# Optimization experiments

Measured on AMD Instinct MI355X. Metric: run time of the kernel, lower is better.

The kernel has to match this reference:

```python
import jax, jax.numpy as jnp
import numpy as np

T, B, IN = 1000, 64, 300          # timesteps, batch, input neurons
A, P = 6, 4                        # num_areas, pop_per_area
L = A * P                          # latent_size = 24
O = 200                            # neurons per area (n_units=1200 / 6 areas)
N_DELAY = 5                        # effective recurrent synaptic delay (steps)
SIGMA = 0.1                        # sigma_mem_noise
TAU = 10.0


def setup_inputs() -> dict:
    key = jax.random.key(0)
    ks = jax.random.split(key, 8)
    x = jax.random.normal(ks[0], (T, B, IN), jnp.float32)
    mem_noise = jax.random.normal(ks[1], (T, B, L), jnp.float32)
    trial_noise = jax.random.uniform(ks[2], (B, 2), jnp.float32) - 0.5
    w_in = jax.random.normal(ks[3], (L, IN), jnp.float32) / np.sqrt(IN)
    w_rec = jax.random.normal(ks[4], (1, L, L), jnp.float32) / np.sqrt(L)
    v_rest = jnp.zeros((L,), jnp.float32)
    bias_noise = jnp.ones((L,), jnp.float32)
    trial_offset_w = (jax.random.uniform(ks[5], (2, L), jnp.float32) - 0.5) / np.sqrt(2.0)
    decay_v = jnp.full((L,), np.exp(-1.0 / TAU), jnp.float32)
    proj_w = jax.random.normal(ks[6], (A, O, P), jnp.float32) / np.sqrt(P)
    proj_b = jnp.zeros((A, O), jnp.float32)
    return dict(x=x, mem_noise=mem_noise, trial_noise=trial_noise, w_in=w_in,
                w_rec=w_rec, v_rest=v_rest, bias_noise=bias_noise,
                trial_offset_w=trial_offset_w, decay_v=decay_v,
                proj_w=proj_w, proj_b=proj_b)


def reference(x, mem_noise, trial_noise, w_in, w_rec, v_rest, bias_noise,
              trial_offset_w, decay_v, proj_w, proj_b):
    # Constant-per-trial offset + input current + resting potential: (T,B,L)
    offset = trial_noise @ trial_offset_w                       # (B,L)
    drive = jnp.einsum('tbi,li->tbl', x, w_in) + offset + v_rest
    noise = SIGMA * bias_noise * mem_noise                      # (T,B,L)
    w_rec0_t = w_rec[0].T                                       # (L,L)

    def step(carry, inp):
        v, buf = carry                 # buf: (N_DELAY,B,L), oldest first
        d, n = inp
        i_rec = buf[0] @ w_rec0_t      # delayed population rate -> current
        v = decay_v * v + (1.0 - decay_v) * (d + i_rec) + n
        rate = jax.nn.sigmoid(v)       # population firing rate
        buf = jnp.concatenate([buf[1:], rate[None]], axis=0)
        return (v, buf), rate

    v0 = jnp.zeros((B, L), x.dtype)
    buf0 = jnp.zeros((N_DELAY, B, L), x.dtype)
    _, rates = jax.lax.scan(step, (v0, buf0), (drive, noise))   # (T,B,L)

    # Per-area projection from population rates to per-neuron rates.
    pop = rates.reshape(T, B, A, P)
    units = jnp.einsum('tbap,aop->tbao', pop, proj_w) + proj_b  # (T,B,A,O)
    return jax.nn.sigmoid(units).reshape(T, B, A * O)
```

## Files before the change

kernel.cpp:

```cpp
#include <hip/hip_runtime.h>

#define T_STEPS 1000
#define BATCH   64
#define IN_N    300
#define L_N     24
#define SIGMA   0.1f
#define RSTR    32

typedef float f32x4 __attribute__((ext_vector_type(4)));

#define WS_G_OFF  8192
#define TBL       (T_STEPS * BATCH * L_N)

__global__ void k0_prep(const float* __restrict__ w_in, const float* __restrict__ w_rec,
                        const float* __restrict__ v_rest, const float* __restrict__ bias_noise,
                        const float* __restrict__ trial_offset_w, const float* __restrict__ decay_v,
                        float* __restrict__ ws) {
    int i = blockIdx.x * 256 + threadIdx.x;
    float* wTs = ws;
    float* Wss = ws + 7200;
    float* ow  = ws + 7776;
    float* c0  = ws + 7824;
    float* snl = ws + 7848;
    if (i < 7200) {
        int k = i / 24, l = i % 24;
        wTs[i] = w_in[l * 300 + k] * (1.f - decay_v[l]);
    } else if (i < 7776) {
        int j = i - 7200; int l = j / 24;
        Wss[j] = w_rec[j] * (1.f - decay_v[l]);
    } else if (i < 7824) {
        int j = i - 7776; int l = j % 24;
        ow[j] = trial_offset_w[j] * (1.f - decay_v[l]);
    } else if (i < 7848) {
        int l = i - 7824;
        c0[l] = v_rest[l] * (1.f - decay_v[l]);
    } else if (i < 7872) {
        int l = i - 7848;
        snl[l] = SIGMA * bias_noise[l];
    }
}

#define K1_ROWS    128
#define K1_THREADS 128
#define KC         60
#define XPITCH     61

__global__ __launch_bounds__(K1_THREADS) void k1_drive(
    const float* __restrict__ x, const float* __restrict__ ws,
    const float* __restrict__ trial_noise, const float* __restrict__ mem_noise,
    float* __restrict__ g) {
    __shared__ float xt[K1_ROWS * XPITCH];
    const float* wTs = ws;
    const float* ow  = ws + 7776;
    const float* c0  = ws + 7824;
    const float* snl = ws + 7848;
    const int tid  = threadIdx.x;
    const int row0 = blockIdx.x * K1_ROWS;

    float acc[L_N];
#pragma unroll
    for (int l = 0; l < L_N; ++l) acc[l] = 0.f;

    const float4* xg = reinterpret_cast<const float4*>(x);
    for (int c = 0; c < IN_N / KC; ++c) {
#pragma unroll
        for (int j = 0; j < 15; ++j) {
            int e4 = tid + j * K1_THREADS;
            int r = e4 / 15, kq = e4 % 15;
            float4 v = xg[(row0 + r) * (IN_N / 4) + c * (KC / 4) + kq];
            float* d = &xt[r * XPITCH + kq * 4];
            d[0] = v.x; d[1] = v.y; d[2] = v.z; d[3] = v.w;
        }
        __syncthreads();
        const float* wrow = wTs + c * KC * L_N;
#pragma unroll 2
        for (int kk = 0; kk < KC; ++kk) {
            float xv = xt[tid * XPITCH + kk];
#pragma unroll
            for (int l = 0; l < L_N; ++l)
                acc[l] = fmaf(xv, wrow[kk * L_N + l], acc[l]);
        }
        __syncthreads();
    }

    const int row = row0 + tid;
    const int b   = row & (BATCH - 1);
    float2 tn = reinterpret_cast<const float2*>(trial_noise)[b];
    const float4* nz = reinterpret_cast<const float4*>(mem_noise + (size_t)row * L_N);
    float4 z[6];
#pragma unroll
    for (int q = 0; q < 6; ++q) z[q] = nz[q];
    float zz[L_N];
#pragma unroll
    for (int q = 0; q < 6; ++q) {
        zz[4*q] = z[q].x; zz[4*q+1] = z[q].y; zz[4*q+2] = z[q].z; zz[4*q+3] = z[q].w;
    }
    float o[L_N];
#pragma unroll
    for (int l = 0; l < L_N; ++l)
        o[l] = acc[l] + tn.x * ow[l] + tn.y * ow[L_N + l] + c0[l] + snl[l] * zz[l];
    float4* dg = reinterpret_cast<float4*>(g + (size_t)row * L_N);
#pragma unroll
    for (int i = 0; i < 6; ++i)
        dg[i] = make_float4(o[4*i], o[4*i+1], o[4*i+2], o[4*i+3]);
}

#define K2_STEP(s, C0, C1, C2, CG) do {                                        \
    float p0 = C0.x * W0.x, p1 = C0.y * W0.y, p2 = C0.z * W0.z, p3 = C0.w * W0.w; \
    p0 = fmaf(C1.x, W1.x, p0); p1 = fmaf(C1.y, W1.y, p1);                      \
    p2 = fmaf(C1.z, W1.z, p2); p3 = fmaf(C1.w, W1.w, p3);                      \
    p0 = fmaf(C2.x, W2.x, p0); p1 = fmaf(C2.y, W2.y, p1);                      \
    p2 = fmaf(C2.z, W2.z, p2); p3 = fmaf(C2.w, W2.w, p3);                      \
    { const float4* q_ = reinterpret_cast<const float4*>(                      \
          &ring[(((s) + 5) & 7) * RSTR + h12]);                                \
      C0 = q_[0]; C1 = q_[1]; C2 = q_[2]; }                                    \
    float pa = (p0 + p1) + (p2 + p3);                                          \
    pa += __shfl_xor(pa, 32);                                                  \
    v = fmaf(dec, v, (CG) + pa);                                               \
    float rate_ = 1.f / (1.f + __expf(-v));                                    \
    if (act) {                                                                 \
        ring[((s) & 7) * RSTR + li] = rate_;                                   \
        rp[(tb + (s)) * (BATCH * L_N)] = rate_;                                \
    }                                                                          \
} while (0)

__global__ __launch_bounds__(64) void k2_scan(
    const float* __restrict__ g, const float* __restrict__ ws,
    const float* __restrict__ decay_v, float* __restrict__ rates) {
    __shared__ __align__(16) float ring[8 * RSTR];
    const float* Wss = ws + 7200;
    const int tid  = threadIdx.x;
    const int b    = blockIdx.x;
    const int half = tid >> 5;
    const int li   = tid & 31;
    const int lc   = (li < 24) ? li : 0;
    const bool act = (li < 24) && (half == 0);
    const int h12  = half * 12;

    const float4* wv = reinterpret_cast<const float4*>(Wss + lc * 24 + h12);
    float4 W0 = wv[0], W1 = wv[1], W2 = wv[2];
    const float dec = decay_v[lc];

    ring[tid] = 0.f; ring[tid + 64] = 0.f; ring[tid + 128] = 0.f; ring[tid + 192] = 0.f;
    __syncthreads();

    const float* gp = g + b * L_N + lc;
    float* rp = rates + b * L_N + lc;

    float cg0 = gp[0 * 1536], cg1 = gp[1 * 1536], cg2 = gp[2 * 1536], cg3 = gp[3 * 1536];
    float cg4 = gp[4 * 1536], cg5 = gp[5 * 1536], cg6 = gp[6 * 1536], cg7 = gp[7 * 1536];

    float v = 0.f;
    float4 A0, A1, A2, B0, B1, B2;
    {
        const float4* q = reinterpret_cast<const float4*>(&ring[3 * RSTR + h12]);
        A0 = q[0]; A1 = q[1]; A2 = q[2];
        q = reinterpret_cast<const float4*>(&ring[4 * RSTR + h12]);
        B0 = q[0]; B1 = q[1]; B2 = q[2];
    }

    for (int tb = 0; tb < T_STEPS - 8; tb += 8) {
        const float* gn = gp + (tb + 8) * 1536;
        float n0 = gn[0 * 1536], n1 = gn[1 * 1536], n2 = gn[2 * 1536], n3 = gn[3 * 1536];
        float n4 = gn[4 * 1536], n5 = gn[5 * 1536], n6 = gn[6 * 1536], n7 = gn[7 * 1536];
        K2_STEP(0, A0, A1, A2, cg0);
        K2_STEP(1, B0, B1, B2, cg1);
        K2_STEP(2, A0, A1, A2, cg2);
        K2_STEP(3, B0, B1, B2, cg3);
        K2_STEP(4, A0, A1, A2, cg4);
        K2_STEP(5, B0, B1, B2, cg5);
        K2_STEP(6, A0, A1, A2, cg6);
        K2_STEP(7, B0, B1, B2, cg7);
        cg0 = n0; cg1 = n1; cg2 = n2; cg3 = n3;
        cg4 = n4; cg5 = n5; cg6 = n6; cg7 = n7;
    }
    {
        const int tb = T_STEPS - 8;
        K2_STEP(0, A0, A1, A2, cg0);
        K2_STEP(1, B0, B1, B2, cg1);
        K2_STEP(2, A0, A1, A2, cg2);
        K2_STEP(3, B0, B1, B2, cg3);
        K2_STEP(4, A0, A1, A2, cg4);
        K2_STEP(5, B0, B1, B2, cg5);
        K2_STEP(6, A0, A1, A2, cg6);
        K2_STEP(7, B0, B1, B2, cg7);
    }
}

#define K3_ROWS 32
__global__ __launch_bounds__(320) void k3_proj(
    const float* __restrict__ rates, const float* __restrict__ proj_w,
    const float* __restrict__ proj_b, float* __restrict__ out) {
    __shared__ float4 lw[1200];
    __shared__ float4 lb[300];
    __shared__ float4 lp[K3_ROWS * 6];
    const int tid  = threadIdx.x;
    const int row0 = blockIdx.x * K3_ROWS;

    const float4* pw4 = reinterpret_cast<const float4*>(proj_w);
    const float4* pb4 = reinterpret_cast<const float4*>(proj_b);
    const float4* rt4 = reinterpret_cast<const float4*>(rates);
    for (int i = tid; i < 1200; i += 320) lw[i] = pw4[i];
    if (tid < 300) lb[tid] = pb4[tid];
    if (tid < K3_ROWS * 6) lp[tid] = rt4[row0 * 6 + tid];
    __syncthreads();

    if (tid < 300) {
        const int a = tid / 50;
        float4 bb = lb[tid];
        float4 w0 = lw[4 * tid], w1 = lw[4 * tid + 1];
        float4 w2 = lw[4 * tid + 2], w3 = lw[4 * tid + 3];
        float4* outp = reinterpret_cast<float4*>(out) + (size_t)row0 * 300 + tid;
#pragma unroll 4
        for (int r = 0; r < K3_ROWS; ++r) {
            float4 p = lp[r * 6 + a];
            float o0 = fmaf(w0.x, p.x, fmaf(w0.y, p.y, fmaf(w0.z, p.z, fmaf(w0.w, p.w, bb.x))));
            float o1 = fmaf(w1.x, p.x, fmaf(w1.y, p.y, fmaf(w1.z, p.z, fmaf(w1.w, p.w, bb.y))));
            float o2 = fmaf(w2.x, p.x, fmaf(w2.y, p.y, fmaf(w2.z, p.z, fmaf(w2.w, p.w, bb.z))));
            float o3 = fmaf(w3.x, p.x, fmaf(w3.y, p.y, fmaf(w3.z, p.z, fmaf(w3.w, p.w, bb.w))));
            f32x4 res;
            res.x = __builtin_amdgcn_rcpf(1.f + __expf(-o0));
            res.y = __builtin_amdgcn_rcpf(1.f + __expf(-o1));
            res.z = __builtin_amdgcn_rcpf(1.f + __expf(-o2));
            res.w = __builtin_amdgcn_rcpf(1.f + __expf(-o3));
            __builtin_nontemporal_store(res, reinterpret_cast<f32x4*>(outp));
            outp += 300;
        }
    }
}

extern "C" void kernel_launch(void* const* d_in, const int* in_sizes, int n_in,
                              void* d_out, int out_size, void* d_ws, size_t ws_size,
                              hipStream_t stream) {
    const float* x              = (const float*)d_in[0];
    const float* mem_noise      = (const float*)d_in[1];
    const float* trial_noise    = (const float*)d_in[2];
    const float* w_in           = (const float*)d_in[3];
    const float* w_rec          = (const float*)d_in[4];
    const float* v_rest         = (const float*)d_in[5];
    const float* bias_noise     = (const float*)d_in[6];
    const float* trial_offset_w = (const float*)d_in[7];
    const float* decay_v        = (const float*)d_in[8];
    const float* proj_w         = (const float*)d_in[9];
    const float* proj_b         = (const float*)d_in[10];
    float* out = (float*)d_out;

    float* ws     = (float*)d_ws;
    float* gbuf   = ws + WS_G_OFF;
    float* ratesb = gbuf + TBL;
    if (ws_size < (size_t)(WS_G_OFF + 2 * TBL) * sizeof(float)) return;

    hipLaunchKernelGGL(k0_prep, dim3(31), dim3(256), 0, stream,
                       w_in, w_rec, v_rest, bias_noise, trial_offset_w, decay_v, ws);
    hipLaunchKernelGGL(k1_drive, dim3((T_STEPS * BATCH) / K1_ROWS), dim3(K1_THREADS),
                       0, stream, x, ws, trial_noise, mem_noise, gbuf);
    hipLaunchKernelGGL(k2_scan, dim3(BATCH), dim3(64), 0, stream,
                       gbuf, ws, decay_v, ratesb);
    hipLaunchKernelGGL(k3_proj, dim3((T_STEPS * BATCH) / K3_ROWS), dim3(320),
                       0, stream, ratesb, proj_w, proj_b, out);
}
```

Before: 560.3 us.

## Process scan in 5-step windows exploiting recurrent delay to batch matvecs

Because the recurrent input uses rates delayed by five steps, the scan kernel now computes five recurrent dot products at once per window, then chains only the cheap decay FMAs serially. Rates are exchanged through a double-buffered LDS block once per window instead of every step, and global rate stores move to the other half-wave. The sigmoid uses a fast reciprocal intrinsic. This shortens the per-step serial dependency chain (LDS read, dot, shuffle) at the cost of more registers and a small loss of reciprocal precision.

```diff
diff --git a/kernel.cpp b/kernel.cpp
--- a/kernel.cpp
+++ b/kernel.cpp
@@ -5,7 +5,6 @@
 #define IN_N    300
 #define L_N     24
 #define SIGMA   0.1f
-#define RSTR    32
 
 typedef float f32x4 __attribute__((ext_vector_type(4)));
 
@@ -105,85 +104,108 @@
         dg[i] = make_float4(o[4*i], o[4*i+1], o[4*i+2], o[4*i+3]);
 }
 
-#define K2_STEP(s, C0, C1, C2, CG) do {                                        \
-    float p0 = C0.x * W0.x, p1 = C0.y * W0.y, p2 = C0.z * W0.z, p3 = C0.w * W0.w; \
-    p0 = fmaf(C1.x, W1.x, p0); p1 = fmaf(C1.y, W1.y, p1);                      \
-    p2 = fmaf(C1.z, W1.z, p2); p3 = fmaf(C1.w, W1.w, p3);                      \
-    p0 = fmaf(C2.x, W2.x, p0); p1 = fmaf(C2.y, W2.y, p1);                      \
-    p2 = fmaf(C2.z, W2.z, p2); p3 = fmaf(C2.w, W2.w, p3);                      \
-    { const float4* q_ = reinterpret_cast<const float4*>(                      \
-          &ring[(((s) + 5) & 7) * RSTR + h12]);                                \
-      C0 = q_[0]; C1 = q_[1]; C2 = q_[2]; }                                    \
-    float pa = (p0 + p1) + (p2 + p3);                                          \
-    pa += __shfl_xor(pa, 32);                                                  \
-    v = fmaf(dec, v, (CG) + pa);                                               \
-    float rate_ = 1.f / (1.f + __expf(-v));                                    \
-    if (act) {                                                                 \
-        ring[((s) & 7) * RSTR + li] = rate_;                                   \
-        rp[(tb + (s)) * (BATCH * L_N)] = rate_;                                \
-    }                                                                          \
+#define K2_DOT(A_, B_, C_, PA_) do {                                           \
+    float p0 = A_.x * W0.x, p1 = A_.y * W0.y, p2 = A_.z * W0.z, p3 = A_.w * W0.w; \
+    p0 = fmaf(B_.x, W1.x, p0); p1 = fmaf(B_.y, W1.y, p1);                      \
+    p2 = fmaf(B_.z, W1.z, p2); p3 = fmaf(B_.w, W1.w, p3);                      \
+    p0 = fmaf(C_.x, W2.x, p0); p1 = fmaf(C_.y, W2.y, p1);                      \
+    p2 = fmaf(C_.z, W2.z, p2); p3 = fmaf(C_.w, W2.w, p3);                      \
+    PA_ = (p0 + p1) + (p2 + p3);                                               \
 } while (0)
+
+#define K2_SIG(v_) __builtin_amdgcn_rcpf(1.f + __expf(-(v_)))
 
 __global__ __launch_bounds__(64) void k2_scan(
     const float* __restrict__ g, const float* __restrict__ ws,
     const float* __restrict__ decay_v, float* __restrict__ rates) {
-    __shared__ __align__(16) float ring[8 * RSTR];
+    __shared__ __align__(16) float ring[320];
     const float* Wss = ws + 7200;
     const int tid  = threadIdx.x;
     const int b    = blockIdx.x;
     const int half = tid >> 5;
     const int li   = tid & 31;
     const int lc   = (li < 24) ? li : 0;
-    const bool act = (li < 24) && (half == 0);
+    const bool actw = (li < 24) && (half == 0);
+    const bool acts = (li < 24) && (half == 1);
     const int h12  = half * 12;
 
     const float4* wv = reinterpret_cast<const float4*>(Wss + lc * 24 + h12);
     float4 W0 = wv[0], W1 = wv[1], W2 = wv[2];
     const float dec = decay_v[lc];
 
-    ring[tid] = 0.f; ring[tid + 64] = 0.f; ring[tid + 128] = 0.f; ring[tid + 192] = 0.f;
-    __syncthreads();
-
     const float* gp = g + b * L_N + lc;
     float* rp = rates + b * L_N + lc;
 
-    float cg0 = gp[0 * 1536], cg1 = gp[1 * 1536], cg2 = gp[2 * 1536], cg3 = gp[3 * 1536];
-    float cg4 = gp[4 * 1536], cg5 = gp[5 * 1536], cg6 = gp[6 * 1536], cg7 = gp[7 * 1536];
+    float4 Z = make_float4(0.f, 0.f, 0.f, 0.f);
+    float4 R00 = Z, R01 = Z, R02 = Z, R10 = Z, R11 = Z, R12 = Z;
+    float4 R20 = Z, R21 = Z, R22 = Z, R30 = Z, R31 = Z, R32 = Z;
+    float4 R40 = Z, R41 = Z, R42 = Z;
+
+    float ga0 = gp[0], ga1 = gp[1536], ga2 = gp[2*1536], ga3 = gp[3*1536], ga4 = gp[4*1536];
+    float gb0 = gp[5*1536], gb1 = gp[6*1536], gb2 = gp[7*1536], gb3 = gp[8*1536], gb4 = gp[9*1536];
 
     float v = 0.f;
-    float4 A0, A1, A2, B0, B1, B2;
-    {
-        const float4* q = reinterpret_cast<const float4*>(&ring[3 * RSTR + h12]);
-        A0 = q[0]; A1 = q[1]; A2 = q[2];
-        q = reinterpret_cast<const float4*>(&ring[4 * RSTR + h12]);
-        B0 = q[0]; B1 = q[1]; B2 = q[2];
-    }
-
-    for (int tb = 0; tb < T_STEPS - 8; tb += 8) {
-        const float* gn = gp + (tb + 8) * 1536;
-        float n0 = gn[0 * 1536], n1 = gn[1 * 1536], n2 = gn[2 * 1536], n3 = gn[3 * 1536];
-        float n4 = gn[4 * 1536], n5 = gn[5 * 1536], n6 = gn[6 * 1536], n7 = gn[7 * 1536];
-        K2_STEP(0, A0, A1, A2, cg0);
-        K2_STEP(1, B0, B1, B2, cg1);
-        K2_STEP(2, A0, A1, A2, cg2);
-        K2_STEP(3, B0, B1, B2, cg3);
-        K2_STEP(4, A0, A1, A2, cg4);
-        K2_STEP(5, B0, B1, B2, cg5);
-        K2_STEP(6, A0, A1, A2, cg6);
-        K2_STEP(7, B0, B1, B2, cg7);
-        cg0 = n0; cg1 = n1; cg2 = n2; cg3 = n3;
-        cg4 = n4; cg5 = n5; cg6 = n6; cg7 = n7;
-    }
-    {
-        const int tb = T_STEPS - 8;
-        K2_STEP(0, A0, A1, A2, cg0);
-        K2_STEP(1, B0, B1, B2, cg1);
-        K2_STEP(2, A0, A1, A2, cg2);
-        K2_STEP(3, B0, B1, B2, cg3);
-        K2_STEP(4, A0, A1, A2, cg4);
-        K2_STEP(5, B0, B1, B2, cg5);
-        K2_STEP(6, A0, A1, A2, cg6);
-        K2_STEP(7, B0, B1, B2, cg7);
+
+    for (int w = 0; w < 200; ++w) {
+        const int t0 = 5 * w;
+        const int tnw = (w < 198) ? (t0 + 10) : 0;
+        const float* gnp = gp + tnw * 1536;
+        float gc0 = gnp[0], gc1 = gnp[1536], gc2 = gnp[2*1536], gc3 = gnp[3*1536], gc4 = gnp[4*1536];
+
+        float pa0, pa1, pa2, pa3, pa4;
+        K2_DOT(R00, R01, R02, pa0);
+        K2_DOT(R10, R11, R12, pa1);
+        K2_DOT(R20, R21, R22, pa2);
+        K2_DOT(R30, R31, R32, pa3);
+        K2_DOT(R40, R41, R42, pa4);
+        pa0 += __shfl_xor(pa0, 32);
+        pa1 += __shfl_xor(pa1, 32);
+        pa2 += __shfl_xor(pa2, 32);
+        pa3 += __shfl_xor(pa3, 32);
+        pa4 += __shfl_xor(pa4, 32);
+
+        float v0 = fmaf(dec, v,  ga0 + pa0);
+        float v1 = fmaf(dec, v0, ga1 + pa1);
+        float v2 = fmaf(dec, v1, ga2 + pa2);
+        float v3 = fmaf(dec, v2, ga3 + pa3);
+        float v4 = fmaf(dec, v3, ga4 + pa4);
+        v = v4;
+
+        float r0 = K2_SIG(v0);
+        float r1 = K2_SIG(v1);
+        float r2 = K2_SIG(v2);
+        float r3 = K2_SIG(v3);
+        float r4 = K2_SIG(v4);
+
+        const int grp = (w & 1) * 160;
+        if (actw) {
+            ring[grp + 0*32 + li] = r0;
+            ring[grp + 1*32 + li] = r1;
+            ring[grp + 2*32 + li] = r2;
+            ring[grp + 3*32 + li] = r3;
+            ring[grp + 4*32 + li] = r4;
+        }
+        {
+            const float4* q0 = reinterpret_cast<const float4*>(&ring[grp + 0*32 + h12]);
+            R00 = q0[0]; R01 = q0[1]; R02 = q0[2];
+            const float4* q1 = reinterpret_cast<const float4*>(&ring[grp + 1*32 + h12]);
+            R10 = q1[0]; R11 = q1[1]; R12 = q1[2];
+            const float4* q2 = reinterpret_cast<const float4*>(&ring[grp + 2*32 + h12]);
+            R20 = q2[0]; R21 = q2[1]; R22 = q2[2];
+            const float4* q3 = reinterpret_cast<const float4*>(&ring[grp + 3*32 + h12]);
+            R30 = q3[0]; R31 = q3[1]; R32 = q3[2];
+            const float4* q4 = reinterpret_cast<const float4*>(&ring[grp + 4*32 + h12]);
+            R40 = q4[0]; R41 = q4[1]; R42 = q4[2];
+        }
+        if (acts) {
+            rp[(t0 + 0) * 1536] = r0;
+            rp[(t0 + 1) * 1536] = r1;
+            rp[(t0 + 2) * 1536] = r2;
+            rp[(t0 + 3) * 1536] = r3;
+            rp[(t0 + 4) * 1536] = r4;
+        }
+        ga0 = gb0; ga1 = gb1; ga2 = gb2; ga3 = gb3; ga4 = gb4;
+        gb0 = gc0; gb1 = gc1; gb2 = gc2; gb3 = gc3; gb4 = gc4;
     }
 }
 
```

Result: faster. 525.4 us (-6.2%).
